# Performance work log

Hardware: AMD Instinct MI355X
Metric: run time of the kernel (lower is better)

The kernel has to match this reference:

```python
import jax, jax.numpy as jnp
import numpy as np

N_ACTIVE = 200000   # active voxels
GRID = 96           # spatial grid extent per axis
C = 128             # inplanes == outplanes
EPS = 1e-4          # scn BatchNormalization default eps


def _build_rulebook(n, g, seed=0):
    """Submanifold 3x3x3 rulebook: for each of 27 offsets, pairs (in_site, out_site)
    where coord[in] = coord[out] + offset and both sites are active. Padded to
    length n with dummy index n."""
    rng = np.random.default_rng(seed)
    lin = rng.choice(g ** 3, size=n, replace=False)
    coords = np.stack(np.unravel_index(lin, (g, g, g)), axis=1)  # [n,3]
    lut = -np.ones(g ** 3, dtype=np.int64)
    lut[lin] = np.arange(n)
    in_rows, out_rows = [], []
    for dx in (-1, 0, 1):
        for dy in (-1, 0, 1):
            for dz in (-1, 0, 1):
                nb = coords + np.array([dx, dy, dz])
                valid = np.all((nb >= 0) & (nb < g), axis=1)
                j = np.full(n, -1, dtype=np.int64)
                j[valid] = lut[np.ravel_multi_index(nb[valid].T, (g, g, g))]
                hit = j >= 0
                ii = j[hit]
                oi = np.nonzero(hit)[0].astype(np.int64)
                pad = n - ii.shape[0]
                in_rows.append(np.concatenate([ii, np.full(pad, n, dtype=np.int64)]))
                out_rows.append(np.concatenate([oi, np.full(pad, n, dtype=np.int64)]))
    return np.stack(in_rows), np.stack(out_rows)  # each [27, n]


def setup_inputs() -> dict:
    key = jax.random.key(0)
    k_feat, k_w1, k_w2 = jax.random.split(key, 3)
    in_idx_np, out_idx_np = _build_rulebook(N_ACTIVE, GRID)
    w_std = 1.0 / np.sqrt(27 * C)
    return {
        "features": jax.random.normal(k_feat, (N_ACTIVE, C), dtype=jnp.float32),
        "W1": jax.random.normal(k_w1, (27, C, C), dtype=jnp.float32) * w_std,
        "gamma1": jnp.ones((C,), jnp.float32),
        "beta1": jnp.zeros((C,), jnp.float32),
        "W2": jax.random.normal(k_w2, (27, C, C), dtype=jnp.float32) * w_std,
        "gamma2": jnp.ones((C,), jnp.float32),
        "beta2": jnp.zeros((C,), jnp.float32),
        "in_idx": jnp.asarray(in_idx_np),
        "out_idx": jnp.asarray(out_idx_np),
    }


def _subm_conv(feats, W, in_idx, out_idx):
    # feats: [N, Cin]; W: [27, Cin, Cout]; rulebook idx: [27, K] (dummy = N)
    n, c_in = feats.shape
    c_out = W.shape[-1]
    feats_pad = jnp.concatenate([feats, jnp.zeros((1, c_in), feats.dtype)], axis=0)

    def step(acc, t):
        ii, oi, w = t
        contrib = feats_pad[ii] @ w  # [K, Cout] gather -> GEMM
        return acc.at[oi].add(contrib), None  # scatter-add (dummy row n absorbs pad)

    acc0 = jnp.zeros((n + 1, c_out), feats.dtype)
    acc, _ = jax.lax.scan(step, acc0, (in_idx, out_idx, W))
    return acc[:n]


def _bn(x, gamma, beta):
    # batch-norm over active sites (training-mode batch stats)
    m = x.mean(axis=0)
    v = x.var(axis=0)
    return (x - m) * jax.lax.rsqrt(v + EPS) * gamma + beta


def reference(features, W1, gamma1, beta1, W2, gamma2, beta2, in_idx, out_idx):
    out = _subm_conv(features, W1, in_idx, out_idx)
    out = jax.nn.relu(_bn(out, gamma1, beta1))          # scn.BatchNormReLU
    out = _subm_conv(out, W2, in_idx, out_idx)
    out = _bn(out, gamma2, beta2)                       # scn.BatchNormalization
    return jax.nn.relu(out + features)                  # AddTable + ReLU
```

## Files before the change

kernel.cpp:

```cpp
#include <hip/hip_runtime.h>

#define NACT 200000
#define MPAD 200064
#define NBLK 1563
#define KOFF 27

#define NB_FILL 21101
#define NB_CAST 25001
#define NB_PREPW 1728
#define NB_PREP (NB_FILL + NB_CAST + NB_PREPW + 1)

typedef __bf16 bf16x8 __attribute__((ext_vector_type(8)));
typedef __bf16 bf16x4 __attribute__((ext_vector_type(4)));
typedef float f32x4 __attribute__((ext_vector_type(4)));

__device__ __forceinline__ void async_load16(const void* g, void* l) {
  __builtin_amdgcn_global_load_lds(
      (__attribute__((address_space(1))) void*)g,
      (__attribute__((address_space(3))) void*)l, 16, 0, 0);
}

__global__ void prep(int* __restrict__ G, const float* __restrict__ F,
                     __bf16* __restrict__ X, const float* __restrict__ W1,
                     const float* __restrict__ W2, __bf16* __restrict__ T1,
                     __bf16* __restrict__ T2, float* __restrict__ st) {
  const int b = blockIdx.x, t = threadIdx.x;
  if (b < NB_FILL) {
    int i = b * 256 + t;
    if (i < KOFF * MPAD) G[i] = NACT;
  } else if (b < NB_FILL + NB_CAST) {
    int i = (b - NB_FILL) * 256 + t;
    if (i >= (NACT + 1) * 32) return;
    float4 v = (i < NACT * 32) ? ((const float4*)F)[i] : make_float4(0.f, 0.f, 0.f, 0.f);
    bf16x4 o = {(__bf16)v.x, (__bf16)v.y, (__bf16)v.z, (__bf16)v.w};
    *(bf16x4*)(X + (i << 2)) = o;
  } else if (b < NB_FILL + NB_CAST + NB_PREPW) {
    int i = (b - NB_FILL - NB_CAST) * 256 + t;
    int k = i >> 14, rem = i & 16383, n = rem >> 7, c = rem & 127;
    int src = (k << 14) + (c << 7) + n;
    T1[i] = (__bf16)W1[src];
    T2[i] = (__bf16)W2[src];
  } else {
    if (t < 512) st[t] = 0.f;
  }
}

__global__ void scatter_g(const int* __restrict__ ii, const int* __restrict__ oi,
                          int* __restrict__ G) {
  int i = blockIdx.x * 256 + threadIdx.x;
  if (i >= KOFF * NACT) return;
  int k = i / NACT;
  int o = oi[i];
  if (o < NACT) G[k * MPAD + o] = ii[i];
}

__global__ __launch_bounds__(256, 4) void gemm_gather(
    const __bf16* __restrict__ X,
    const __bf16* __restrict__ WT,
    const int* __restrict__ G,
    __bf16* __restrict__ Y,
    float* __restrict__ st)
{
  __shared__ __bf16 Alds[128 * 64];
  __shared__ __bf16 Blds[128 * 64];
  const int t = threadIdx.x;
  const int lane = t & 63;
  const int w = t >> 6;
  const int wm = (w & 1) << 6;
  const int wn = (w >> 1) << 6;
  const int m_base = blockIdx.x << 7;
  const int r0 = t >> 3;
  const int scb = t & 7;
  const int l15 = lane & 15;
  const int q4 = lane >> 4;

  f32x4 acc[4][4];
#pragma unroll
  for (int i = 0; i < 4; ++i)
#pragma unroll
    for (int j = 0; j < 4; ++j) acc[i][j] = (f32x4){0.f, 0.f, 0.f, 0.f};

  for (int kk = 0; kk < KOFF; ++kk) {
    int rowA[4];
#pragma unroll
    for (int j = 0; j < 4; ++j)
      rowA[j] = G[kk * MPAD + m_base + r0 + j * 32];
    const __bf16* wb = WT + (kk << 14);
#pragma unroll
    for (int s = 0; s < 2; ++s) {
      const int c0 = s << 6;
      __syncthreads();
#pragma unroll
      for (int j = 0; j < 4; ++j) {
        const int r = r0 + j * 32;
        const int gcb = scb ^ (r & 7);
        async_load16(wb + (r << 7) + c0 + (gcb << 3), &Blds[(((r << 3) + scb) << 3)]);
        async_load16(X + ((size_t)rowA[j] << 7) + c0 + (gcb << 3),
                     &Alds[(((r << 3) + scb) << 3)]);
      }
      __syncthreads();
#pragma unroll
      for (int ks = 0; ks < 2; ++ks) {
        bf16x8 af[4], bfr[4];
        const int cb0 = (ks << 2) + q4;
#pragma unroll
        for (int mi = 0; mi < 4; ++mi) {
          const int r = wm + mi * 16 + l15;
          af[mi] = *(const bf16x8*)&Alds[(((r << 3) + (cb0 ^ (r & 7))) << 3)];
        }
#pragma unroll
        for (int ni = 0; ni < 4; ++ni) {
          const int r = wn + ni * 16 + l15;
          bfr[ni] = *(const bf16x8*)&Blds[(((r << 3) + (cb0 ^ (r & 7))) << 3)];
        }
#pragma unroll
        for (int mi = 0; mi < 4; ++mi)
#pragma unroll
          for (int ni = 0; ni < 4; ++ni)
            acc[mi][ni] = __builtin_amdgcn_mfma_f32_16x16x32_bf16(
                af[mi], bfr[ni], acc[mi][ni], 0, 0, 0);
      }
    }
  }

#pragma unroll
  for (int mi = 0; mi < 4; ++mi) {
#pragma unroll
    for (int ni = 0; ni < 4; ++ni) {
      const int col = wn + ni * 16 + l15;
#pragma unroll
      for (int rg = 0; rg < 4; ++rg) {
        const int row = m_base + wm + mi * 16 + (q4 << 2) + rg;
        Y[(row << 7) + col] = (__bf16)acc[mi][ni][rg];
      }
    }
  }

  float s[4], s2[4];
#pragma unroll
  for (int ni = 0; ni < 4; ++ni) {
    float a = 0.f, b = 0.f;
#pragma unroll
    for (int mi = 0; mi < 4; ++mi)
#pragma unroll
      for (int rg = 0; rg < 4; ++rg) {
        float v = acc[mi][ni][rg];
        a += v; b += v * v;
      }
    s[ni] = a; s2[ni] = b;
  }
#pragma unroll
  for (int ni = 0; ni < 4; ++ni) {
    s[ni]  += __shfl_xor(s[ni], 16);  s[ni]  += __shfl_xor(s[ni], 32);
    s2[ni] += __shfl_xor(s2[ni], 16); s2[ni] += __shfl_xor(s2[ni], 32);
  }
  float* sc = (float*)Alds;
  __syncthreads();
  if (q4 == 0) {
#pragma unroll
    for (int ni = 0; ni < 4; ++ni) {
      sc[(w << 6) + ni * 16 + l15]       = s[ni];
      sc[256 + (w << 6) + ni * 16 + l15] = s2[ni];
    }
  }
  __syncthreads();
  {
    const int kind = t >> 7, col = t & 127;
    const int w1 = (col >> 6) << 1;
    const float v = sc[kind * 256 + (w1 << 6) + (col & 63)] +
                    sc[kind * 256 + ((w1 + 1) << 6) + (col & 63)];
    atomicAdd(&st[t], v);
  }
}

__global__ void bn_relu_cast(const __bf16* __restrict__ Y, const float* __restrict__ st,
                             const float* __restrict__ gamma, const float* __restrict__ beta,
                             __bf16* __restrict__ X2) {
  __shared__ float co[256];
  const int t = threadIdx.x;
  if (t < 128) {
    float m = st[t] * (1.f / NACT);
    float v = st[128 + t] * (1.f / NACT) - m * m;
    float sc = gamma[t] * rsqrtf(v + 1e-4f);
    co[t] = sc;
    co[128 + t] = beta[t] - m * sc;
  }
  __syncthreads();
  int i = blockIdx.x * 256 + t;
  if (i >= (NACT + 1) * 16) return;
  bf16x8 o;
  if (i < NACT * 16) {
    bf16x8 v = ((const bf16x8*)Y)[i];
    int cg = (i & 15) << 3;
#pragma unroll
    for (int e = 0; e < 8; ++e) {
      float x = fmaf((float)v[e], co[cg + e], co[128 + cg + e]);
      o[e] = (__bf16)fmaxf(x, 0.f);
    }
  } else {
#pragma unroll
    for (int e = 0; e < 8; ++e) o[e] = (__bf16)0.f;
  }
  ((bf16x8*)X2)[i] = o;
}

__global__ void bn_add_relu(const __bf16* __restrict__ Y, const float* __restrict__ st,
                            const float* __restrict__ gamma, const float* __restrict__ beta,
                            const float* __restrict__ F, float* __restrict__ O) {
  __shared__ float co[256];
  const int t = threadIdx.x;
  if (t < 128) {
    float m = st[t] * (1.f / NACT);
    float v = st[128 + t] * (1.f / NACT) - m * m;
    float sc = gamma[t] * rsqrtf(v + 1e-4f);
    co[t] = sc;
    co[128 + t] = beta[t] - m * sc;
  }
  __syncthreads();
  int i = blockIdx.x * 256 + t;
  if (i >= NACT * 16) return;
  bf16x8 v = ((const bf16x8*)Y)[i];
  float4 f0 = ((const float4*)F)[2 * i];
  float4 f1 = ((const float4*)F)[2 * i + 1];
  int cg = (i & 15) << 3;
  float4 o0, o1;
  o0.x = fmaxf(fmaf((float)v[0], co[cg + 0], co[128 + cg + 0]) + f0.x, 0.f);
  o0.y = fmaxf(fmaf((float)v[1], co[cg + 1], co[128 + cg + 1]) + f0.y, 0.f);
  o0.z = fmaxf(fmaf((float)v[2], co[cg + 2], co[128 + cg + 2]) + f0.z, 0.f);
  o0.w = fmaxf(fmaf((float)v[3], co[cg + 3], co[128 + cg + 3]) + f0.w, 0.f);
  o1.x = fmaxf(fmaf((float)v[4], co[cg + 4], co[128 + cg + 4]) + f1.x, 0.f);
  o1.y = fmaxf(fmaf((float)v[5], co[cg + 5], co[128 + cg + 5]) + f1.y, 0.f);
  o1.z = fmaxf(fmaf((float)v[6], co[cg + 6], co[128 + cg + 6]) + f1.z, 0.f);
  o1.w = fmaxf(fmaf((float)v[7], co[cg + 7], co[128 + cg + 7]) + f1.w, 0.f);
  ((float4*)O)[2 * i] = o0;
  ((float4*)O)[2 * i + 1] = o1;
}

extern "C" void kernel_launch(void* const* d_in, const int* in_sizes, int n_in,
                              void* d_out, int out_size, void* d_ws, size_t ws_size,
                              hipStream_t stream) {
  const float* features = (const float*)d_in[0];
  const float* W1       = (const float*)d_in[1];
  const float* gamma1   = (const float*)d_in[2];
  const float* beta1    = (const float*)d_in[3];
  const float* W2       = (const float*)d_in[4];
  const float* gamma2   = (const float*)d_in[5];
  const float* beta2    = (const float*)d_in[6];
  const int* in_idx     = (const int*)d_in[7];
  const int* out_idx    = (const int*)d_in[8];

  char* ws = (char*)d_ws;
  size_t off = 0;
  int*    G   = (int*)(ws + off);    off += (size_t)KOFF * MPAD * 4;
  __bf16* X   = (__bf16*)(ws + off); off += (size_t)(NACT + 1) * 128 * 2;
  __bf16* T1  = (__bf16*)(ws + off); off += (size_t)KOFF * 128 * 128 * 2;
  __bf16* T2  = (__bf16*)(ws + off); off += (size_t)KOFF * 128 * 128 * 2;
  __bf16* Y   = (__bf16*)(ws + off); off += (size_t)MPAD * 128 * 2;
  float*  st  = (float*)(ws + off);  off += 4096;

  prep<<<NB_PREP, 256, 0, stream>>>(G, features, X, W1, W2, T1, T2, st);
  scatter_g<<<(KOFF * NACT + 255) / 256, 256, 0, stream>>>(in_idx, out_idx, G);

  gemm_gather<<<NBLK, 256, 0, stream>>>(X, T1, G, Y, st);
  bn_relu_cast<<<((NACT + 1) * 16 + 255) / 256, 256, 0, stream>>>(Y, st, gamma1, beta1, X);

  gemm_gather<<<NBLK, 256, 0, stream>>>(X, T2, G, Y, st + 256);
  bn_add_relu<<<(NACT * 16 + 255) / 256, 256, 0, stream>>>(Y, st + 256, gamma2, beta2,
                                                           features, (float*)d_out);
}
```

Measured before the change: 612.4 us.

## Build gather table per output tile via binary search; transpose weights through LDS

```diff
diff --git a/kernel.cpp b/kernel.cpp
--- a/kernel.cpp
+++ b/kernel.cpp
@@ -5,10 +5,9 @@
 #define NBLK 1563
 #define KOFF 27
 
-#define NB_FILL 21101
 #define NB_CAST 25001
-#define NB_PREPW 1728
-#define NB_PREP (NB_FILL + NB_CAST + NB_PREPW + 1)
+#define NB_PREP (NB_CAST + 1)
+#define GB_PER_K 196
 
 typedef __bf16 bf16x8 __attribute__((ext_vector_type(8)));
 typedef __bf16 bf16x4 __attribute__((ext_vector_type(4)));
@@ -20,38 +19,78 @@
       (__attribute__((address_space(3))) void*)l, 16, 0, 0);
 }
 
-__global__ void prep(int* __restrict__ G, const float* __restrict__ F,
-                     __bf16* __restrict__ X, const float* __restrict__ W1,
-                     const float* __restrict__ W2, __bf16* __restrict__ T1,
-                     __bf16* __restrict__ T2, float* __restrict__ st) {
+__global__ void prep(const float* __restrict__ F, __bf16* __restrict__ X,
+                     float* __restrict__ st) {
   const int b = blockIdx.x, t = threadIdx.x;
-  if (b < NB_FILL) {
+  if (b < NB_CAST) {
     int i = b * 256 + t;
-    if (i < KOFF * MPAD) G[i] = NACT;
-  } else if (b < NB_FILL + NB_CAST) {
-    int i = (b - NB_FILL) * 256 + t;
     if (i >= (NACT + 1) * 32) return;
     float4 v = (i < NACT * 32) ? ((const float4*)F)[i] : make_float4(0.f, 0.f, 0.f, 0.f);
     bf16x4 o = {(__bf16)v.x, (__bf16)v.y, (__bf16)v.z, (__bf16)v.w};
     *(bf16x4*)(X + (i << 2)) = o;
-  } else if (b < NB_FILL + NB_CAST + NB_PREPW) {
-    int i = (b - NB_FILL - NB_CAST) * 256 + t;
-    int k = i >> 14, rem = i & 16383, n = rem >> 7, c = rem & 127;
-    int src = (k << 14) + (c << 7) + n;
-    T1[i] = (__bf16)W1[src];
-    T2[i] = (__bf16)W2[src];
   } else {
     if (t < 512) st[t] = 0.f;
   }
 }
 
-__global__ void scatter_g(const int* __restrict__ ii, const int* __restrict__ oi,
-                          int* __restrict__ G) {
-  int i = blockIdx.x * 256 + threadIdx.x;
-  if (i >= KOFF * NACT) return;
-  int k = i / NACT;
-  int o = oi[i];
-  if (o < NACT) G[k * MPAD + o] = ii[i];
+__global__ void wtrans(const float* __restrict__ W1, const float* __restrict__ W2,
+                       __bf16* __restrict__ T1, __bf16* __restrict__ T2) {
+  __shared__ __bf16 tile[128 * 129];
+  const int k = blockIdx.x, t = threadIdx.x;
+#pragma unroll
+  for (int m = 0; m < 2; ++m) {
+    const float4* w = (const float4*)((m ? W2 : W1) + (k << 14));
+    __bf16* T = (m ? T2 : T1) + (k << 14);
+    if (m) __syncthreads();
+#pragma unroll
+    for (int j = 0; j < 16; ++j) {
+      int base = (j << 10) + (t << 2);
+      int c = base >> 7, n = base & 127;
+      float4 v = w[(j << 8) + t];
+      tile[(n + 0) * 129 + c] = (__bf16)v.x;
+      tile[(n + 1) * 129 + c] = (__bf16)v.y;
+      tile[(n + 2) * 129 + c] = (__bf16)v.z;
+      tile[(n + 3) * 129 + c] = (__bf16)v.w;
+    }
+    __syncthreads();
+#pragma unroll
+    for (int j = 0; j < 16; ++j) {
+      int base = (j << 10) + (t << 2);
+      int n = base >> 7, c = base & 127;
+      bf16x4 o = {tile[n * 129 + c], tile[n * 129 + c + 1],
+                  tile[n * 129 + c + 2], tile[n * 129 + c + 3]};
+      *(bf16x4*)(T + base) = o;
+    }
+  }
+}
+
+__global__ __launch_bounds__(256) void build_g(const int* __restrict__ ii,
+                                               const int* __restrict__ oi,
+                                               int* __restrict__ G) {
+  __shared__ int buf[1024];
+  const int b = blockIdx.x;
+  const int k = b / GB_PER_K;
+  const int bo = b - k * GB_PER_K;
+  const int o0 = bo << 10;
+  const int t = threadIdx.x;
+  buf[t] = NACT; buf[t + 256] = NACT; buf[t + 512] = NACT; buf[t + 768] = NACT;
+  const int* ok = oi + (size_t)k * NACT;
+  int lo = 0, hi = NACT;
+  while (lo < hi) { int mid = (lo + hi) >> 1; if (ok[mid] < o0) lo = mid + 1; else hi = mid; }
+  const int s = lo;
+  int lo2 = s, hi2 = NACT;
+  const int tgt = o0 + 1024;
+  while (lo2 < hi2) { int mid = (lo2 + hi2) >> 1; if (ok[mid] < tgt) lo2 = mid + 1; else hi2 = mid; }
+  const int e = lo2;
+  __syncthreads();
+  for (int p = s + t; p < e; p += 256) {
+    int o = ok[p] - o0;
+    buf[o] = ii[(size_t)k * NACT + p];
+  }
+  __syncthreads();
+  const int idx = o0 + (t << 2);
+  if (idx < MPAD)
+    *(int4*)(G + (size_t)k * MPAD + idx) = *(const int4*)(buf + (t << 2));
 }
 
 __global__ __launch_bounds__(256, 4) void gemm_gather(
@@ -258,8 +297,9 @@
   __bf16* Y   = (__bf16*)(ws + off); off += (size_t)MPAD * 128 * 2;
   float*  st  = (float*)(ws + off);  off += 4096;
 
-  prep<<<NB_PREP, 256, 0, stream>>>(G, features, X, W1, W2, T1, T2, st);
-  scatter_g<<<(KOFF * NACT + 255) / 256, 256, 0, stream>>>(in_idx, out_idx, G);
+  prep<<<NB_PREP, 256, 0, stream>>>(features, X, st);
+  wtrans<<<KOFF, 256, 0, stream>>>(W1, W2, T1, T2);
+  build_g<<<KOFF * GB_PER_K, 256, 0, stream>>>(in_idx, out_idx, G);
 
   gemm_gather<<<NBLK, 256, 0, stream>>>(X, T1, G, Y, st);
   bn_relu_cast<<<((NACT + 1) * 16 + 255) / 256, 256, 0, stream>>>(Y, st, gamma1, beta1, X);
```

Measured after the change: 703.1 us. +14.8%, slower.
